# Performance work log

Hardware: AMD Instinct MI355X
Metric: run time of the kernel (lower is better)

Reference implementation:

```python
import jax, jax.numpy as jnp
import numpy as np

D_MODEL = 1024
NUM_HEADS = 16
HEAD_DIM = D_MODEL // NUM_HEADS


def setup_inputs() -> dict:
    key = jax.random.key(0)
    ks = jax.random.split(key, 11)
    B, S = 4, 2048
    scale = 1.0 / np.sqrt(D_MODEL)
    inp = {
        "k": jax.random.normal(ks[0], (B, S, D_MODEL), jnp.float32),
        "q": jax.random.normal(ks[1], (B, S, D_MODEL), jnp.float32),
        "v": jax.random.normal(ks[2], (B, S, D_MODEL), jnp.float32),
        "w_k": jax.random.normal(ks[3], (D_MODEL, D_MODEL), jnp.float32) * scale,
        "b_k": jnp.zeros((D_MODEL,), jnp.float32),
        "w_q": jax.random.normal(ks[4], (D_MODEL, D_MODEL), jnp.float32) * scale,
        "b_q": jnp.zeros((D_MODEL,), jnp.float32),
        "w_v": jax.random.normal(ks[5], (D_MODEL, D_MODEL), jnp.float32) * scale,
        "b_v": jnp.zeros((D_MODEL,), jnp.float32),
        "w_o": jax.random.normal(ks[6], (D_MODEL, D_MODEL), jnp.float32) * scale,
        "b_o": jnp.zeros((D_MODEL,), jnp.float32),
    }
    return inp


def _split_heads(x):
    B, S, _ = x.shape
    return x.reshape(B, S, NUM_HEADS, HEAD_DIM).transpose(0, 2, 1, 3)  # [B,H,S,Dh]


def reference(k, q, v, w_k, b_k, w_q, b_q, w_v, b_v, w_o, b_o):
    # Linear projections (torch Linear: x @ W.T + b; here weights stored as [in,out])
    kp = k @ w_k + b_k
    qp = q @ w_q + b_q
    vp = v @ w_v + b_v
    kh = _split_heads(kp)
    qh = _split_heads(qp)
    vh = _split_heads(vp)
    # NOTE: original divides by head_dim, not sqrt(head_dim)
    scores = jnp.einsum("bhsd,bhtd->bhst", qh, kh) / HEAD_DIM
    attn = jax.nn.softmax(scores, axis=-1)
    # dropout is identity in eval mode (deterministic baseline)
    ctx = jnp.einsum("bhst,bhtd->bhsd", attn, vh)
    B, H, S, Dh = ctx.shape
    ctx = ctx.transpose(0, 2, 1, 3).reshape(B, S, D_MODEL)
    return ctx @ w_o + b_o
```

## Files before the change

### kernel.cpp

```cpp
#include <hip/hip_runtime.h>

#define D_MODEL 1024
#define S_LEN   2048
#define BATCH   4
#define NHEAD   16
#define HDIM    64
#define NTOK    (BATCH * S_LEN)

typedef __attribute__((ext_vector_type(8))) __bf16 bf16x8;
typedef __attribute__((ext_vector_type(4))) float  floatx4;

static __device__ inline floatx4 mfma16(bf16x8 a, bf16x8 b, floatx4 c) {
    return __builtin_amdgcn_mfma_f32_16x16x32_bf16(a, b, c, 0, 0, 0);
}

static __device__ inline void gload_lds16(const __bf16* g, __bf16* l) {
    __builtin_amdgcn_global_load_lds(
        (const __attribute__((address_space(1))) void*)g,
        (__attribute__((address_space(3))) void*)l, 16, 0, 0);
}

#define BARRIER()   asm volatile("s_barrier" ::: "memory")
#define WAITVM4()   asm volatile("s_waitcnt vmcnt(4)" ::: "memory")
#define WAITLGKM8() asm volatile("s_waitcnt lgkmcnt(8)" ::: "memory")

#if __has_builtin(__builtin_amdgcn_exp2f)
#define EXP2(x) __builtin_amdgcn_exp2f(x)
#else
#define EXP2(x) exp2f(x)
#endif

static __device__ inline unsigned pack_bf16(float a, float b) {
    unsigned ua = __builtin_bit_cast(unsigned, a) + 0x8000u;
    unsigned ub = __builtin_bit_cast(unsigned, b) + 0x8000u;
#if __has_builtin(__builtin_amdgcn_perm)
    return __builtin_amdgcn_perm(ub, ua, 0x07060302u);
#else
    return (ua >> 16) | (ub & 0xffff0000u);
#endif
}

__global__ __launch_bounds__(256) void cvt_qkv(const float* __restrict__ k,
                                               const float* __restrict__ q,
                                               const float* __restrict__ v,
                                               __bf16* __restrict__ kb,
                                               __bf16* __restrict__ qb,
                                               __bf16* __restrict__ vb) {
    const float* x = (blockIdx.y == 0) ? k : (blockIdx.y == 1) ? q : v;
    __bf16* y = (blockIdx.y == 0) ? kb : (blockIdx.y == 1) ? qb : vb;
    size_t i = ((size_t)blockIdx.x * 256 + threadIdx.x) * 8;
    float4 a = *(const float4*)(x + i);
    float4 b = *(const float4*)(x + i + 4);
    bf16x8 o;
    o[0] = (__bf16)a.x; o[1] = (__bf16)a.y; o[2] = (__bf16)a.z; o[3] = (__bf16)a.w;
    o[4] = (__bf16)b.x; o[5] = (__bf16)b.y; o[6] = (__bf16)b.z; o[7] = (__bf16)b.w;
    *(bf16x8*)(y + i) = o;
}

__global__ __launch_bounds__(256) void cvt_w4(const float* __restrict__ w0,
                                              const float* __restrict__ w1,
                                              const float* __restrict__ w2,
                                              const float* __restrict__ w3,
                                              __bf16* __restrict__ t0,
                                              __bf16* __restrict__ t1,
                                              __bf16* __restrict__ t2,
                                              __bf16* __restrict__ t3) {
    const int z = blockIdx.z;
    const float* W = (z == 0) ? w0 : (z == 1) ? w1 : (z == 2) ? w2 : w3;
    __bf16* Wt = (z == 0) ? t0 : (z == 1) ? t1 : (z == 2) ? t2 : t3;
    __shared__ __bf16 t[64][72];
    const int i0 = blockIdx.x * 64;
    const int j0 = blockIdx.y * 64;
    const int tid = threadIdx.x;
    const int r4 = tid >> 4, c4 = (tid & 15) * 4;
#pragma unroll
    for (int rr = 0; rr < 64; rr += 16) {
        int r = rr + r4;
        float4 v = *(const float4*)(W + (size_t)(i0 + r) * D_MODEL + j0 + c4);
        t[c4 + 0][r] = (__bf16)v.x;
        t[c4 + 1][r] = (__bf16)v.y;
        t[c4 + 2][r] = (__bf16)v.z;
        t[c4 + 3][r] = (__bf16)v.w;
    }
    __syncthreads();
    const int r8 = tid >> 3, c8 = (tid & 7) * 8;
#pragma unroll
    for (int rr = 0; rr < 64; rr += 32) {
        int r = rr + r8;
        bf16x8 o;
#pragma unroll
        for (int e = 0; e < 8; e++) o[e] = t[r][c8 + e];
        *(bf16x8*)(Wt + (size_t)(j0 + r) * D_MODEL + i0 + c8) = o;
    }
}

#define BM 128
#define BN 128
#define BK 64
template <int OUT_F32>
__device__ __forceinline__ void gemm_body(const __bf16* __restrict__ A,
                                          const __bf16* __restrict__ Bt,
                                          void* __restrict__ Cp,
                                          const float* __restrict__ biasN,
                                          const float* __restrict__ biasM,
                                          int N, int K, float scale,
                                          int bm, int bn,
                                          __bf16* lA, __bf16* lB) {
    const int tid = threadIdx.x;
    const int wave = tid >> 6, lane = tid & 63;
    const int quad = lane >> 4, l16 = lane & 15;
    const int swz = l16 & 7;
    const int wm = (wave >> 1) * 64, wn = (wave & 1) * 64;

    floatx4 acc[4][4];
#pragma unroll
    for (int i = 0; i < 4; i++)
#pragma unroll
        for (int j = 0; j < 4; j++) acc[i][j] = (floatx4){0.f, 0.f, 0.f, 0.f};

    const __bf16* Ag = A + (size_t)bm * K;
    const __bf16* Bg = Bt + (size_t)bn * K;

    for (int k0 = 0; k0 < K; k0 += BK) {
        __syncthreads();
#pragma unroll
        for (int i = 0; i < 4; i++) {
            int g = i * 256 + tid;
            int row = g >> 3, cl = (g & 7) ^ (row & 7);
            gload_lds16(Ag + (size_t)row * K + k0 + cl * 8, lA + g * 8);
            gload_lds16(Bg + (size_t)row * K + k0 + cl * 8, lB + g * 8);
        }
        __syncthreads();
#pragma unroll
        for (int kk = 0; kk < 2; kk++) {
            bf16x8 af[4], bf[4];
#pragma unroll
            for (int i = 0; i < 4; i++) {
                int ra = wm + i * 16 + l16, rb = wn + i * 16 + l16;
                af[i] = *(const bf16x8*)(lA + ra * BK + ((kk * 4 + quad) ^ swz) * 8);
                bf[i] = *(const bf16x8*)(lB + rb * BK + ((kk * 4 + quad) ^ swz) * 8);
            }
#pragma unroll
            for (int i = 0; i < 4; i++)
#pragma unroll
                for (int j = 0; j < 4; j++) acc[i][j] = mfma16(af[i], bf[j], acc[i][j]);
        }
    }

#pragma unroll
    for (int i = 0; i < 4; i++) {
#pragma unroll
        for (int r = 0; r < 4; r++) {
            int row = bm + wm + i * 16 + quad * 4 + r;
            float brow = biasM ? biasM[row] : 0.0f;
#pragma unroll
            for (int j = 0; j < 4; j++) {
                int col = bn + wn + j * 16 + l16;
                float v = (acc[i][j][r] + brow + (biasN ? biasN[col] : 0.0f)) * scale;
                if constexpr (OUT_F32)
                    ((float*)Cp)[(size_t)row * N + col] = v;
                else
                    ((__bf16*)Cp)[(size_t)row * N + col] = (__bf16)v;
            }
        }
    }
}

__global__ __launch_bounds__(256, 3) void qkv_gemm(const __bf16* __restrict__ kb,
                                                   const __bf16* __restrict__ qb,
                                                   const __bf16* __restrict__ vb,
                                                   const __bf16* __restrict__ WtK,
                                                   const __bf16* __restrict__ WtQ,
                                                   const __bf16* __restrict__ WtV,
                                                   __bf16* Kp, __bf16* Qp, __bf16* Vtp,
                                                   const float* b_k, const float* b_q,
                                                   const float* b_v, float qscale) {
    __shared__ __bf16 lA[BM * BK];
    __shared__ __bf16 lB[BN * BK];
    const int z = blockIdx.z;
    if (z == 0)
        gemm_body<0>(kb, WtK, Kp, b_k, nullptr, D_MODEL, D_MODEL, 1.0f,
                     blockIdx.x * BM, blockIdx.y * BN, lA, lB);
    else if (z == 1)
        gemm_body<0>(qb, WtQ, Qp, b_q, nullptr, D_MODEL, D_MODEL, qscale,
                     blockIdx.x * BM, blockIdx.y * BN, lA, lB);
    else
        gemm_body<0>(WtV, vb, Vtp, nullptr, b_v, NTOK, D_MODEL, 1.0f,
                     blockIdx.y * BM, blockIdx.x * BN, lA, lB);
}

__global__ __launch_bounds__(256, 3) void out_gemm(const __bf16* __restrict__ A,
                                                   const __bf16* __restrict__ Bt,
                                                   float* __restrict__ C,
                                                   const float* __restrict__ biasN) {
    __shared__ __bf16 lA[BM * BK];
    __shared__ __bf16 lB[BN * BK];
    gemm_body<1>(A, Bt, C, biasN, nullptr, D_MODEL, D_MODEL, 1.0f,
                 blockIdx.x * BM, blockIdx.y * BN, lA, lB);
}

#define QT_M 256
#define KVT  64

template <int CUR>
__device__ __forceinline__ void attn_step(
    __bf16 (&lK)[2][KVT * HDIM], __bf16 (&lV)[2][HDIM * KVT], __bf16* lPw,
    const __bf16* Kg, const __bf16* Vg, int t0n,
    const bf16x8 (&qf)[4][2], floatx4 (&octx)[4][4], float2 (&lsum2)[4],
    int tid, int quad, int l16, int swz) {
    constexpr int NXT = CUR ^ 1;

    BARRIER();
#pragma unroll
    for (int i = 0; i < 2; i++) {
        int g = i * 256 + tid;
        int row = g >> 3, cl = (g & 7) ^ (row & 7);
        gload_lds16(Kg + (size_t)(t0n + row) * D_MODEL + cl * 8, &lK[NXT][g * 8]);
        gload_lds16(Vg + (size_t)row * NTOK + t0n + cl * 8, &lV[NXT][g * 8]);
    }
    WAITVM4();
    BARRIER();

#pragma unroll
    for (int half = 0; half < 2; half++) {
#pragma unroll
        for (int tt2 = 0; tt2 < 2; tt2++) {
            const int tt = half * 2 + tt2;
            bf16x8 kf0 = *(const bf16x8*)(&lK[CUR][(tt * 16 + l16) * HDIM + ((0 + quad) ^ swz) * 8]);
            bf16x8 kf1 = *(const bf16x8*)(&lK[CUR][(tt * 16 + l16) * HDIM + ((4 + quad) ^ swz) * 8]);
            floatx4 sc[4];
#pragma unroll
            for (int m = 0; m < 4; m++) {
                sc[m] = mfma16(kf0, qf[m][0], (floatx4){0.f, 0.f, 0.f, 0.f});
                sc[m] = mfma16(kf1, qf[m][1], sc[m]);
            }
            int c = tt * 4 + quad;
            int g = c >> 1, hf = c & 1;
            int off = ((g ^ swz) * 8 + hf * 4);
#pragma unroll
            for (int m = 0; m < 4; m++) {
                float p0 = EXP2(sc[m][0]), p1 = EXP2(sc[m][1]);
                float p2 = EXP2(sc[m][2]), p3 = EXP2(sc[m][3]);
                lsum2[m].x += p0 + p1;
                lsum2[m].y += p2 + p3;
                unsigned lo = pack_bf16(p0, p1), hi = pack_bf16(p2, p3);
                *(uint2*)(lPw + (m * 16 + l16) * 64 + off) = make_uint2(lo, hi);
            }
        }
    }

#pragma unroll
    for (int kh = 0; kh < 2; kh++) {
        WAITLGKM8();
        int goff = (((kh << 2) | quad) ^ swz) * 8;
        bf16x8 vf[4], pf[4];
#pragma unroll
        for (int j = 0; j < 4; j++)
            vf[j] = *(const bf16x8*)(&lV[CUR][(j * 16 + l16) * KVT + goff]);
#pragma unroll
        for (int m = 0; m < 4; m++)
            pf[m] = *(const bf16x8*)(lPw + (m * 16 + l16) * 64 + goff);
#pragma unroll
        for (int m = 0; m < 4; m++)
#pragma unroll
            for (int j = 0; j < 4; j++)
                octx[m][j] = mfma16(pf[m], vf[j], octx[m][j]);
    }
}

__global__ __launch_bounds__(256, 2) void attn(const __bf16* __restrict__ Qp,
                                               const __bf16* __restrict__ Kp,
                                               const __bf16* __restrict__ Vt,
                                               __bf16* __restrict__ ctx) {
    const int qt = blockIdx.x, h = blockIdx.y, b = blockIdx.z;
    const int tid = threadIdx.x;
    const int wave = tid >> 6, lane = tid & 63;
    const int quad = lane >> 4, l16 = lane & 15;
    const int swz = l16 & 7;

    __shared__ __bf16 lK[2][KVT * HDIM];
    __shared__ __bf16 lV[2][HDIM * KVT];
    __shared__ __bf16 lP[4][64 * 64];

    const int qbase = b * S_LEN + qt * QT_M + wave * 64;
    bf16x8 qf[4][2];
#pragma unroll
    for (int m = 0; m < 4; m++)
#pragma unroll
        for (int hf = 0; hf < 2; hf++)
            qf[m][hf] = *(const bf16x8*)(Qp + (size_t)(qbase + m * 16 + l16) * D_MODEL +
                                         h * HDIM + hf * 32 + quad * 8);

    floatx4 octx[4][4];
    float2 lsum2[4];
#pragma unroll
    for (int m = 0; m < 4; m++) {
#pragma unroll
        for (int j = 0; j < 4; j++) octx[m][j] = (floatx4){0.f, 0.f, 0.f, 0.f};
        lsum2[m] = make_float2(0.f, 0.f);
    }

    const __bf16* Kg = Kp + (size_t)(b * S_LEN) * D_MODEL + h * HDIM;
    const __bf16* Vg = Vt + (size_t)(h * HDIM) * NTOK + (size_t)b * S_LEN;

#pragma unroll
    for (int i = 0; i < 2; i++) {
        int g = i * 256 + tid;
        int row = g >> 3, cl = (g & 7) ^ (row & 7);
        gload_lds16(Kg + (size_t)row * D_MODEL + cl * 8, &lK[0][g * 8]);
        gload_lds16(Vg + (size_t)row * NTOK + cl * 8, &lV[0][g * 8]);
    }

    __bf16* lPw = &lP[wave][0];

    for (int it2 = 0; it2 < S_LEN / KVT / 2; ++it2) {
        attn_step<0>(lK, lV, lPw, Kg, Vg, (2 * it2 + 1) * KVT,
                     qf, octx, lsum2, tid, quad, l16, swz);
        attn_step<1>(lK, lV, lPw, Kg, Vg, ((2 * it2 + 2) * KVT) & (S_LEN - 1),
                     qf, octx, lsum2, tid, quad, l16, swz);
    }

#pragma unroll
    for (int m = 0; m < 4; m++) {
        float l = lsum2[m].x + lsum2[m].y;
        l += __shfl_xor(l, 16, 64);
        l += __shfl_xor(l, 32, 64);
#pragma unroll
        for (int r = 0; r < 4; r++) {
            float linv = 1.0f / __shfl(l, quad * 4 + r, 64);
            int qrow = qbase + m * 16 + quad * 4 + r;
#pragma unroll
            for (int j = 0; j < 4; j++) {
                int col = h * HDIM + j * 16 + l16;
                ctx[(size_t)qrow * D_MODEL + col] = (__bf16)(octx[m][j][r] * linv);
            }
        }
    }
}

extern "C" void kernel_launch(void* const* d_in, const int* in_sizes, int n_in,
                              void* d_out, int out_size, void* d_ws, size_t ws_size,
                              hipStream_t stream) {
    (void)in_sizes; (void)n_in; (void)out_size; (void)ws_size;
    const float* k_in = (const float*)d_in[0];
    const float* q_in = (const float*)d_in[1];
    const float* v_in = (const float*)d_in[2];
    const float* w_k  = (const float*)d_in[3];
    const float* b_k  = (const float*)d_in[4];
    const float* w_q  = (const float*)d_in[5];
    const float* b_q  = (const float*)d_in[6];
    const float* w_v  = (const float*)d_in[7];
    const float* b_v  = (const float*)d_in[8];
    const float* w_o  = (const float*)d_in[9];
    const float* b_o  = (const float*)d_in[10];

    char* ws = (char*)d_ws;
    const size_t SZ = (size_t)NTOK * D_MODEL * sizeof(__bf16);
    __bf16* kb  = (__bf16*)(ws + 0 * SZ);
    __bf16* qb  = (__bf16*)(ws + 1 * SZ);
    __bf16* vb  = (__bf16*)(ws + 2 * SZ);
    __bf16* WtK = (__bf16*)(ws + 3 * SZ);
    __bf16* WtQ = WtK + (size_t)D_MODEL * D_MODEL;
    __bf16* WtV = WtQ + (size_t)D_MODEL * D_MODEL;
    __bf16* WtO = WtV + (size_t)D_MODEL * D_MODEL;
    __bf16* Kp  = (__bf16*)(ws + 3 * SZ + 4 * (size_t)D_MODEL * D_MODEL * sizeof(__bf16));
    __bf16* Qp  = Kp + (size_t)NTOK * D_MODEL;
    __bf16* Vtp = Qp + (size_t)NTOK * D_MODEL;
    __bf16* ctx = kb;

    const float QSCALE = 1.44269504f / 64.0f;

    cvt_qkv<<<dim3(NTOK * D_MODEL / (256 * 8), 3), 256, 0, stream>>>(
        k_in, q_in, v_in, kb, qb, vb);
    cvt_w4<<<dim3(16, 16, 4), 256, 0, stream>>>(w_k, w_q, w_v, w_o, WtK, WtQ, WtV, WtO);

    qkv_gemm<<<dim3(64, 8, 3), 256, 0, stream>>>(kb, qb, vb, WtK, WtQ, WtV,
                                                 Kp, Qp, Vtp, b_k, b_q, b_v, QSCALE);

    attn<<<dim3(S_LEN / QT_M, NHEAD, BATCH), 256, 0, stream>>>(Qp, Kp, Vtp, ctx);

    out_gemm<<<dim3(64, 8), 256, 0, stream>>>(ctx, WtO, (float*)d_out, b_o);
}
```

Before: 342.2 us.

## Double-buffer GEMM LDS tiles with async prefetch and halve BK

Restructures the projection and output GEMMs to use double-buffered LDS tiles, issuing global-to-LDS loads for the next K slice before computing on the current one. BK drops from 64 to 32 so the two buffers fit in about the same LDS, and launch bounds rise to 4 blocks per CU. The aim is to overlap memory latency with MFMA work instead of stalling on a sync after each load. The cost is more barriers per unit of work and a wrap-around redundant prefetch on the last step. A vmcnt(0) drain is added before the epilogues, including in attention.

```diff
diff --git a/kernel.cpp b/kernel.cpp
--- a/kernel.cpp
+++ b/kernel.cpp
@@ -22,6 +22,7 @@
 
 #define BARRIER()   asm volatile("s_barrier" ::: "memory")
 #define WAITVM4()   asm volatile("s_waitcnt vmcnt(4)" ::: "memory")
+#define WAITVM0()   asm volatile("s_waitcnt vmcnt(0)" ::: "memory")
 #define WAITLGKM8() asm volatile("s_waitcnt lgkmcnt(8)" ::: "memory")
 
 #if __has_builtin(__builtin_amdgcn_exp2f)
@@ -96,7 +97,46 @@
 
 #define BM 128
 #define BN 128
-#define BK 64
+#define BK 32
+
+struct GemmState {
+    floatx4 acc[4][4];
+    const __bf16 *Ag, *Bg;
+    int K;
+};
+
+template <int CUR>
+__device__ __forceinline__ void gemm_step(GemmState& st, __bf16 (&lA)[2][BM * BK],
+                                          __bf16 (&lB)[2][BN * BK], int knext,
+                                          int tid, int quad, int l16) {
+    constexpr int NXT = CUR ^ 1;
+    const int wave = tid >> 6;
+    const int wm = (wave >> 1) * 64, wn = (wave & 1) * 64;
+
+    BARRIER();
+#pragma unroll
+    for (int i = 0; i < 2; i++) {
+        int g = i * 256 + tid;
+        int row = g >> 2, cl = (g & 3) ^ (row & 3);
+        gload_lds16(st.Ag + (size_t)row * st.K + knext + cl * 8, lA[NXT] + g * 8);
+        gload_lds16(st.Bg + (size_t)row * st.K + knext + cl * 8, lB[NXT] + g * 8);
+    }
+    WAITVM4();
+    BARRIER();
+
+    bf16x8 af[4], bf[4];
+    const int ph = (quad ^ (l16 & 3)) * 8;
+#pragma unroll
+    for (int i = 0; i < 4; i++) {
+        af[i] = *(const bf16x8*)(lA[CUR] + (wm + i * 16 + l16) * BK + ph);
+        bf[i] = *(const bf16x8*)(lB[CUR] + (wn + i * 16 + l16) * BK + ph);
+    }
+#pragma unroll
+    for (int i = 0; i < 4; i++)
+#pragma unroll
+        for (int j = 0; j < 4; j++) st.acc[i][j] = mfma16(af[i], bf[j], st.acc[i][j]);
+}
+
 template <int OUT_F32>
 __device__ __forceinline__ void gemm_body(const __bf16* __restrict__ A,
                                           const __bf16* __restrict__ Bt,
@@ -105,47 +145,36 @@
                                           const float* __restrict__ biasM,
                                           int N, int K, float scale,
                                           int bm, int bn,
-                                          __bf16* lA, __bf16* lB) {
+                                          __bf16 (&lA)[2][BM * BK],
+                                          __bf16 (&lB)[2][BN * BK]) {
     const int tid = threadIdx.x;
     const int wave = tid >> 6, lane = tid & 63;
     const int quad = lane >> 4, l16 = lane & 15;
-    const int swz = l16 & 7;
     const int wm = (wave >> 1) * 64, wn = (wave & 1) * 64;
 
-    floatx4 acc[4][4];
+    GemmState st;
 #pragma unroll
     for (int i = 0; i < 4; i++)
 #pragma unroll
-        for (int j = 0; j < 4; j++) acc[i][j] = (floatx4){0.f, 0.f, 0.f, 0.f};
-
-    const __bf16* Ag = A + (size_t)bm * K;
-    const __bf16* Bg = Bt + (size_t)bn * K;
-
-    for (int k0 = 0; k0 < K; k0 += BK) {
-        __syncthreads();
-#pragma unroll
-        for (int i = 0; i < 4; i++) {
-            int g = i * 256 + tid;
-            int row = g >> 3, cl = (g & 7) ^ (row & 7);
-            gload_lds16(Ag + (size_t)row * K + k0 + cl * 8, lA + g * 8);
-            gload_lds16(Bg + (size_t)row * K + k0 + cl * 8, lB + g * 8);
-        }
-        __syncthreads();
-#pragma unroll
-        for (int kk = 0; kk < 2; kk++) {
-            bf16x8 af[4], bf[4];
-#pragma unroll
-            for (int i = 0; i < 4; i++) {
-                int ra = wm + i * 16 + l16, rb = wn + i * 16 + l16;
-                af[i] = *(const bf16x8*)(lA + ra * BK + ((kk * 4 + quad) ^ swz) * 8);
-                bf[i] = *(const bf16x8*)(lB + rb * BK + ((kk * 4 + quad) ^ swz) * 8);
-            }
-#pragma unroll
-            for (int i = 0; i < 4; i++)
-#pragma unroll
-                for (int j = 0; j < 4; j++) acc[i][j] = mfma16(af[i], bf[j], acc[i][j]);
-        }
-    }
+        for (int j = 0; j < 4; j++) st.acc[i][j] = (floatx4){0.f, 0.f, 0.f, 0.f};
+    st.Ag = A + (size_t)bm * K;
+    st.Bg = Bt + (size_t)bn * K;
+    st.K = K;
+
+#pragma unroll
+    for (int i = 0; i < 2; i++) {
+        int g = i * 256 + tid;
+        int row = g >> 2, cl = (g & 3) ^ (row & 3);
+        gload_lds16(st.Ag + (size_t)row * K + cl * 8, lA[0] + g * 8);
+        gload_lds16(st.Bg + (size_t)row * K + cl * 8, lB[0] + g * 8);
+    }
+
+    const int kmask = K - 1;
+    for (int k0 = 0; k0 < K; k0 += 2 * BK) {
+        gemm_step<0>(st, lA, lB, (k0 + BK) & kmask, tid, quad, l16);
+        gemm_step<1>(st, lA, lB, (k0 + 2 * BK) & kmask, tid, quad, l16);
+    }
+    WAITVM0();
 
 #pragma unroll
     for (int i = 0; i < 4; i++) {
@@ -156,7 +185,7 @@
 #pragma unroll
             for (int j = 0; j < 4; j++) {
                 int col = bn + wn + j * 16 + l16;
-                float v = (acc[i][j][r] + brow + (biasN ? biasN[col] : 0.0f)) * scale;
+                float v = (st.acc[i][j][r] + brow + (biasN ? biasN[col] : 0.0f)) * scale;
                 if constexpr (OUT_F32)
                     ((float*)Cp)[(size_t)row * N + col] = v;
                 else
@@ -166,7 +195,7 @@
     }
 }
 
-__global__ __launch_bounds__(256, 3) void qkv_gemm(const __bf16* __restrict__ kb,
+__global__ __launch_bounds__(256, 4) void qkv_gemm(const __bf16* __restrict__ kb,
                                                    const __bf16* __restrict__ qb,
                                                    const __bf16* __restrict__ vb,
                                                    const __bf16* __restrict__ WtK,
@@ -175,8 +204,8 @@
                                                    __bf16* Kp, __bf16* Qp, __bf16* Vtp,
                                                    const float* b_k, const float* b_q,
                                                    const float* b_v, float qscale) {
-    __shared__ __bf16 lA[BM * BK];
-    __shared__ __bf16 lB[BN * BK];
+    __shared__ __bf16 lA[2][BM * BK];
+    __shared__ __bf16 lB[2][BN * BK];
     const int z = blockIdx.z;
     if (z == 0)
         gemm_body<0>(kb, WtK, Kp, b_k, nullptr, D_MODEL, D_MODEL, 1.0f,
@@ -189,12 +218,12 @@
                      blockIdx.y * BM, blockIdx.x * BN, lA, lB);
 }
 
-__global__ __launch_bounds__(256, 3) void out_gemm(const __bf16* __restrict__ A,
+__global__ __launch_bounds__(256, 4) void out_gemm(const __bf16* __restrict__ A,
                                                    const __bf16* __restrict__ Bt,
                                                    float* __restrict__ C,
                                                    const float* __restrict__ biasN) {
-    __shared__ __bf16 lA[BM * BK];
-    __shared__ __bf16 lB[BN * BK];
+    __shared__ __bf16 lA[2][BM * BK];
+    __shared__ __bf16 lB[2][BN * BK];
     gemm_body<1>(A, Bt, C, biasN, nullptr, D_MODEL, D_MODEL, 1.0f,
                  blockIdx.x * BM, blockIdx.y * BN, lA, lB);
 }
@@ -319,6 +348,7 @@
         attn_step<1>(lK, lV, lPw, Kg, Vg, ((2 * it2 + 2) * KVT) & (S_LEN - 1),
                      qf, octx, lsum2, tid, quad, l16, swz);
     }
+    WAITVM0();
 
 #pragma unroll
     for (int m = 0; m < 4; m++) {
```

After: 352.1 us. 2.9% more time.
